# Optimization experiments

Measured on AMD Instinct MI355X. Metric: run time of the kernel, lower is better.

## Reference

```python
import jax, jax.numpy as jnp
import numpy as np

B, C, H, W = 64, 256, 64, 64
E = 4                      # num_experts
CELL = 8
OUT = CELL * CELL + 1      # 65
EPS_BN = 1e-5
EPS_LB = 1e-6


def setup_inputs() -> dict:
    key = jax.random.key(0)
    ks = jax.random.split(key, 6)
    x = jax.random.normal(ks[0], (B, C, H, W), dtype=jnp.float32)
    w_experts = jax.random.normal(ks[1], (E, C, OUT), dtype=jnp.float32) * 0.05
    b_experts = jax.random.normal(ks[2], (E, OUT), dtype=jnp.float32) * 0.05
    w_gate = jax.random.normal(ks[3], (C, E), dtype=jnp.float32) * 0.05
    b_gate = jax.random.normal(ks[4], (E,), dtype=jnp.float32) * 0.05
    gamma = jnp.ones((OUT,), dtype=jnp.float32)
    beta = jnp.zeros((OUT,), dtype=jnp.float32)
    return {"x": x, "w_experts": w_experts, "b_experts": b_experts,
            "w_gate": w_gate, "b_gate": b_gate, "gamma": gamma, "beta": beta}


def pixel_shuffle(t, r):
    n, ch, h, w = t.shape
    nc = ch // (r * r)
    t = t.reshape(n, nc, r, r, h, w)
    t = t.transpose(0, 1, 4, 2, 5, 3)
    return t.reshape(n, nc, h * r, w * r)


def reference(x, w_experts, b_experts, w_gate, b_gate, gamma, beta):
    x = jax.nn.relu(x)
    xh = x.transpose(0, 2, 3, 1)                       # [B,H,W,C]

    # gating: global-avg-pool -> linear -> softmax -> hard top-1
    pooled = xh.mean(axis=(1, 2))                      # [B,C]
    gate = jax.nn.softmax(pooled @ w_gate + b_gate, axis=-1)
    idx = jnp.argmax(gate, axis=-1)                    # [B]

    # load-balancing KL(usage || uniform)
    usage = jnp.mean(jax.nn.one_hot(idx, E, dtype=xh.dtype), axis=0) + EPS_LB
    usage = usage / usage.sum()
    lb_loss = jnp.sum(usage * (jnp.log(usage) - jnp.log(jnp.full_like(usage, 1.0 / E))))

    # fused gather->grouped-GEMM (per-sample expert weight selection)
    w_sel = w_experts[idx]                             # [B,C,OUT]
    b_sel = b_experts[idx]                             # [B,OUT]
    y = jnp.einsum('bhwc,bco->bhwo', xh, w_sel) + b_sel[:, None, None, :]
    y = y.transpose(0, 3, 1, 2)                        # [B,OUT,H,W]

    # BatchNorm2d (training mode: batch statistics, biased variance)
    mean = y.mean(axis=(0, 2, 3), keepdims=True)
    var = y.var(axis=(0, 2, 3), keepdims=True)
    logits = (y - mean) / jnp.sqrt(var + EPS_BN)
    logits = logits * gamma[None, :, None, None] + beta[None, :, None, None]

    prob = jax.nn.softmax(logits, axis=1)[:, :-1]      # drop dustbin channel
    prob = pixel_shuffle(prob, CELL)                   # [B,1,H*8,W*8]
    prob = prob[:, 0]                                  # squeeze dim=1
    return logits, prob, lb_loss
```

## Files before the change

### kernel.cpp

```cpp
#include <hip/hip_runtime.h>
#include <stdint.h>
#include <math.h>

#define B_    64
#define C_    256
#define HW_   4096
#define E_    4
#define OUT_  65
#define NPAD_ 80
#define NSPREAD_ 16

#define LOGITS_SZ (B_*OUT_*HW_)
#define PROB_SZ   (B_*512*512)

#define POOLED_OFF 0u
#define BNS_OFF    65536u
#define BNSS_OFF   70656u
#define CLEAR_BYTES 75776u
#define WT_OFF     75776u
#define YB_OFF     239616u

typedef float  f4 __attribute__((ext_vector_type(4)));
typedef short  s8 __attribute__((ext_vector_type(8)));

__device__ __forceinline__ uint32_t f2bf(float f){
  uint32_t u = __float_as_uint(f);
  return (u + 0x7FFFu + ((u >> 16) & 1u)) >> 16;
}
__device__ __forceinline__ uint32_t pk(float lo, float hi){
  return f2bf(lo) | (f2bf(hi) << 16);
}
__device__ __forceinline__ float bf2f(uint32_t u){
  return __uint_as_float((u & 0xFFFFu) << 16);
}


__global__ __launch_bounds__(256) void k_prep(const float* __restrict__ x,
                                              const float* __restrict__ w_experts,
                                              uint16_t* __restrict__ xb,
                                              uint16_t* __restrict__ Wt,
                                              float* __restrict__ pooled){
  __shared__ float pool_lds[64];
  int bid = blockIdx.x;
  int t = threadIdx.x;

  if (bid >= 8192){
    if (t >= 32) return;
    int pid = bid - 8192;
    int e = pid / NPAD_, o = pid % NPAD_;
    int ks = t >> 2, quad = t & 3;
    int c = t*8;
    float a[8];
    if (o < OUT_){
      const float* src = w_experts + (size_t)e*C_*OUT_ + o;
#pragma unroll
      for (int j = 0; j < 8; ++j) a[j] = src[(size_t)(c+j)*OUT_];
    } else {
#pragma unroll
      for (int j = 0; j < 8; ++j) a[j] = 0.f;
    }
    uint4 wv;
    wv.x = pk(a[0],a[1]); wv.y = pk(a[2],a[3]);
    wv.z = pk(a[4],a[5]); wv.w = pk(a[6],a[7]);
    uint16_t* dst = Wt + ((((size_t)(e*5 + (o>>4))*8 + ks)*64)
                          + (size_t)((o&15)*4 + quad))*8;
    *(uint4*)dst = wv;
    return;
  }

  int b = bid >> 7, ct = (bid >> 5) & 3, pt = bid & 31;
  int cg_ = t & 7, pgg = t >> 3;
  int c0 = ct*64 + cg_*8;
  int p0 = pt*128 + pgg*4;
  if (t < 64) pool_lds[t] = 0.f;
  __syncthreads();

  float v[8][4]; float s[8];
  const float* xp = x + ((size_t)(b*C_ + c0))*HW_ + p0;
#pragma unroll
  for (int r = 0; r < 8; ++r){
    float4 f = *(const float4*)(xp + (size_t)r*HW_);
    v[r][0]=fmaxf(f.x,0.f); v[r][1]=fmaxf(f.y,0.f);
    v[r][2]=fmaxf(f.z,0.f); v[r][3]=fmaxf(f.w,0.f);
    s[r] = v[r][0]+v[r][1]+v[r][2]+v[r][3];
  }
  int ksg  = ct*2 + (cg_ >> 2);
  int quad = cg_ & 3;
  uint16_t* dst0 = xb + ((((size_t)(b*256 + (p0>>4))*8 + ksg)*64)
                         + (size_t)((p0&15)*4 + quad))*8;
#pragma unroll
  for (int pp = 0; pp < 4; ++pp){
    uint4 w;
    w.x = pk(v[0][pp], v[1][pp]); w.y = pk(v[2][pp], v[3][pp]);
    w.z = pk(v[4][pp], v[5][pp]); w.w = pk(v[6][pp], v[7][pp]);
    *(uint4*)(dst0 + pp*32) = w;
  }
#pragma unroll
  for (int r = 0; r < 8; ++r){
    float vv = s[r];
    vv += __shfl_xor(vv, 8);
    vv += __shfl_xor(vv, 16);
    vv += __shfl_xor(vv, 32);
    if ((t & 56) == 0)
      atomicAdd(&pool_lds[cg_*8 + r], vv);
  }
  __syncthreads();
  if (t < 64) atomicAdd(pooled + b*C_ + ct*64 + t, pool_lds[t]);
}

__global__ __launch_bounds__(256) void k_gemm(const uint16_t* __restrict__ xb,
                                              const uint16_t* __restrict__ Wt,
                                              const float* __restrict__ pooled,
                                              const float* __restrict__ w_gate,
                                              const float* __restrict__ b_gate,
                                              const float* __restrict__ b_experts,
                                              uint16_t* __restrict__ yb,
                                              float* __restrict__ bnsum,
                                              float* __restrict__ bnss){
  __shared__ float2 bnp[NPAD_*4];
  __shared__ float glog[4];
  __shared__ int esh;
  int bid = blockIdx.x;
  int b = bid >> 5, pt = bid & 31;
  int t = threadIdx.x;
  int w = t >> 6, lane = t & 63;
  int l15 = lane & 15, quad = lane >> 4;
  int lid = l15*4 + quad;

  if (t < 4){
    float dot = 0.f;
    const float* pr = pooled + b*C_;
    for (int c = 0; c < C_; c += 4){
      float4 p4 = *(const float4*)(pr + c);
      dot += p4.x*w_gate[c*4+t] + p4.y*w_gate[(c+1)*4+t]
           + p4.z*w_gate[(c+2)*4+t] + p4.w*w_gate[(c+3)*4+t];
    }
    glog[t] = dot * (1.f/4096.f) + b_gate[t];
  }
  __syncthreads();
  if (t == 0){
    float best = glog[0]; int bi = 0;
#pragma unroll
    for (int ee = 1; ee < 4; ++ee){ float vv = glog[ee]; if (vv > best){best = vv; bi = ee;} }
    esh = bi;
  }
  __syncthreads();
  int e = esh;

  int p0 = pt*128 + w*32;
  const uint16_t* ap = xb + ((size_t)(b*256 + pt*8 + w*2))*4096 + (size_t)lid*8;
  const uint16_t* bp = Wt + (size_t)e*5*4096 + (size_t)lid*8;

  f4 acc[2][5];
#pragma unroll
  for (int mt=0; mt<2; ++mt)
#pragma unroll
    for (int nt=0; nt<5; ++nt){ f4 z = {0.f,0.f,0.f,0.f}; acc[mt][nt] = z; }

#pragma unroll
  for (int ks = 0; ks < 8; ++ks){
    s8 bv[5];
#pragma unroll
    for (int nt=0; nt<5; ++nt) bv[nt] = *(const s8*)(bp + (size_t)nt*4096 + ks*512);
#pragma unroll
    for (int mt=0; mt<2; ++mt){
      s8 av = *(const s8*)(ap + (size_t)mt*4096 + ks*512);
#pragma unroll
      for (int nt=0; nt<5; ++nt)
        acc[mt][nt] = __builtin_amdgcn_mfma_f32_16x16x32_bf16(av, bv[nt], acc[mt][nt], 0, 0, 0);
    }
  }

#pragma unroll
  for (int nt=0; nt<5; ++nt){
    int o = nt*16 + l15;
    float bias = (o < OUT_) ? b_experts[e*OUT_ + o] : 0.f;
    float s1 = 0.f, s2 = 0.f;
#pragma unroll
    for (int mt=0; mt<2; ++mt){
#pragma unroll
      for (int r=0; r<4; ++r){
        float vv = acc[mt][nt][r] + bias;
        acc[mt][nt][r] = vv;
        s1 += vv; s2 += vv*vv;
      }
      if (o < OUT_){
        size_t base = ((size_t)(b*OUT_ + o))*HW_ + p0 + mt*16 + quad*4;
        uint2 st;
        st.x = pk(acc[mt][nt][0], acc[mt][nt][1]);
        st.y = pk(acc[mt][nt][2], acc[mt][nt][3]);
        *(uint2*)(yb + base) = st;
      }
    }
    s1 += __shfl_xor(s1, 16); s1 += __shfl_xor(s1, 32);
    s2 += __shfl_xor(s2, 16); s2 += __shfl_xor(s2, 32);
    if (quad == 0) bnp[(nt*16 + l15)*4 + w] = make_float2(s1, s2);
  }
  __syncthreads();
  if (t < OUT_){
    float2 a0 = bnp[t*4+0], a1 = bnp[t*4+1], a2 = bnp[t*4+2], a3 = bnp[t*4+3];
    atomicAdd(bnsum + (bid & (NSPREAD_-1))*NPAD_ + t, a0.x+a1.x+a2.x+a3.x);
    atomicAdd(bnss  + (bid & (NSPREAD_-1))*NPAD_ + t, a0.y+a1.y+a2.y+a3.y);
  }
}

__global__ __launch_bounds__(256) void k_final(const uint16_t* __restrict__ yb,
                                               const float* __restrict__ bnsum,
                                               const float* __restrict__ bnss,
                                               const float* __restrict__ gamma,
                                               const float* __restrict__ beta,
                                               const float* __restrict__ pooled,
                                               const float* __restrict__ w_gate,
                                               const float* __restrict__ b_gate,
                                               float* __restrict__ out_logits,
                                               float* __restrict__ out_prob,
                                               float* __restrict__ out_lb){
  __shared__ float lt[OUT_*132];
  __shared__ float2 ss[OUT_];
  __shared__ float sden[256];
  __shared__ float gl[64][4];
  __shared__ int ish[64];
  int bid = blockIdx.x;
  int b = bid >> 5, pt = bid & 31;
  int p0 = pt*128;
  int t = threadIdx.x;
  if (t < OUT_){
    float s1 = 0.f, s2 = 0.f;
#pragma unroll
    for (int k = 0; k < NSPREAD_; ++k){ s1 += bnsum[k*NPAD_ + t]; s2 += bnss[k*NPAD_ + t]; }
    const float invN = 1.f/(float)(B_*HW_);
    float mean = s1*invN;
    float var  = s2*invN - mean*mean;
    float sc   = gamma[t] / sqrtf(var + 1e-5f);
    ss[t] = make_float2(sc, beta[t] - mean*sc);
  }
  __syncthreads();

  int prr = t & 15, og = t >> 4;
#pragma unroll
  for (int oi = 0; oi < 5; ++oi){
    int o = og + oi*16;
    if (o < OUT_){
      size_t base = ((size_t)(b*OUT_ + o))*HW_ + p0 + prr*8;
      uint4 raw = *(const uint4*)(yb + base);
      float f[8];
      f[0]=bf2f(raw.x); f[1]=bf2f(raw.x>>16);
      f[2]=bf2f(raw.y); f[3]=bf2f(raw.y>>16);
      f[4]=bf2f(raw.z); f[5]=bf2f(raw.z>>16);
      f[6]=bf2f(raw.w); f[7]=bf2f(raw.w>>16);
      float2 sv = ss[o];
#pragma unroll
      for (int k=0;k<8;++k) f[k] = f[k]*sv.x + sv.y;
      float4 w0 = make_float4(f[0],f[1],f[2],f[3]);
      float4 w1 = make_float4(f[4],f[5],f[6],f[7]);
      *(float4*)(out_logits + base)     = w0;
      *(float4*)(out_logits + base + 4) = w1;
      float* lp = lt + o*132 + prr*8;
      *(float4*)(lp)     = w0;
      *(float4*)(lp + 4) = w1;
    }
  }
  __syncthreads();

  int px = t & 127, hf = t >> 7;
  {
    int obeg = hf ? 33 : 0, oend = hf ? OUT_ : 33;
    float ssum = 0.f;
    for (int o = obeg; o < oend; ++o){
      float ev = __expf(lt[o*132 + px]);
      lt[o*132 + px] = ev;
      ssum += ev;
    }
    sden[hf*128 + px] = ssum;
  }
  __syncthreads();
  {
    float inv = 1.f/(sden[px] + sden[128 + px]);
    int P = p0 + px;
    int hh = P >> 6, wd = P & 63;
    float* pb = out_prob + ((size_t)b << 18) + (size_t)(hh*8)*512 + (size_t)wd*8;
#pragma unroll
    for (int r1i = 0; r1i < 4; ++r1i){
      int r1 = hf*4 + r1i;
      float4 q0, q1;
      q0.x = lt[(r1*8+0)*132+px]*inv;
      q0.y = lt[(r1*8+1)*132+px]*inv;
      q0.z = lt[(r1*8+2)*132+px]*inv;
      q0.w = lt[(r1*8+3)*132+px]*inv;
      q1.x = lt[(r1*8+4)*132+px]*inv;
      q1.y = lt[(r1*8+5)*132+px]*inv;
      q1.z = lt[(r1*8+6)*132+px]*inv;
      q1.w = lt[(r1*8+7)*132+px]*inv;
      *(float4*)(pb + (size_t)r1*512)     = q0;
      *(float4*)(pb + (size_t)r1*512 + 4) = q1;
    }
  }

  if (bid == 0){
    __syncthreads();
    int bb = t >> 2, ee = t & 3;
    float dot = 0.f;
    const float* pr = pooled + bb*C_;
    for (int c = 0; c < C_; c += 4){
      float4 p4 = *(const float4*)(pr + c);
      dot += p4.x*w_gate[c*4+ee] + p4.y*w_gate[(c+1)*4+ee]
           + p4.z*w_gate[(c+2)*4+ee] + p4.w*w_gate[(c+3)*4+ee];
    }
    gl[bb][ee] = dot * (1.f/4096.f) + b_gate[ee];
    __syncthreads();
    if (t < 64){
      float best = gl[t][0]; int bi = 0;
#pragma unroll
      for (int e2 = 1; e2 < 4; ++e2){ float vv = gl[t][e2]; if (vv > best){best = vv; bi = e2;} }
      ish[t] = bi;
    }
    __syncthreads();
    if (t == 0){
      int cnt[4] = {0,0,0,0};
      for (int b2 = 0; b2 < 64; ++b2) cnt[ish[b2]]++;
      double u[4], S = 0.0;
      for (int e2 = 0; e2 < 4; ++e2){ u[e2] = cnt[e2]/64.0 + 1e-6; S += u[e2]; }
      double lbv = 0.0;
      for (int e2 = 0; e2 < 4; ++e2){ double uu = u[e2]/S; lbv += uu*(log(uu) - log(0.25)); }
      *out_lb = (float)lbv;
    }
  }
}

extern "C" void kernel_launch(void* const* d_in, const int* in_sizes, int n_in,
                              void* d_out, int out_size, void* d_ws, size_t ws_size,
                              hipStream_t stream){
  const float* x         = (const float*)d_in[0];
  const float* w_experts = (const float*)d_in[1];
  const float* b_experts = (const float*)d_in[2];
  const float* w_gate    = (const float*)d_in[3];
  const float* b_gate    = (const float*)d_in[4];
  const float* gamma     = (const float*)d_in[5];
  const float* beta      = (const float*)d_in[6];

  float* out = (float*)d_out;
  char*  ws  = (char*)d_ws;
  float*     pooled = (float*)(ws + POOLED_OFF);
  float*     bnsum  = (float*)(ws + BNS_OFF);
  float*     bnss   = (float*)(ws + BNSS_OFF);
  uint16_t*  Wt     = (uint16_t*)(ws + WT_OFF);
  uint16_t*  ybm    = (uint16_t*)(ws + YB_OFF);
  uint16_t*  xbm    = (uint16_t*)d_out;

  float* logits = out;
  float* prob   = out + LOGITS_SZ;
  float* lbp    = out + LOGITS_SZ + PROB_SZ;

  hipMemsetAsync(ws, 0, CLEAR_BYTES, stream);
  k_prep <<<8512, 256, 0, stream>>>(x, w_experts, xbm, Wt, pooled);
  k_gemm <<<2048, 256, 0, stream>>>(xbm, Wt, pooled, w_gate, b_gate, b_experts,
                                    ybm, bnsum, bnss);
  k_final<<<2048, 256, 0, stream>>>(ybm, bnsum, bnss, gamma, beta,
                                    pooled, w_gate, b_gate, logits, prob, lbp);
}
```

Measured before the change: 488.2 us.

## Drop memset, write partial pools, nontemporal I/O, bf16 LDS staging in final

Replaces global atomic pooling with per-tile partial sums that each GEMM block reduces, so the separate memset launch can go. The BN accumulators are now zeroed inside the prep kernel. The expert choice is stored once per sample, so the final kernel no longer recomputes gating. Input loads and output stores use nontemporal hints, and the softmax staging buffer in LDS is kept as bf16 instead of fp32. Storing exponentials in bf16 lowers prob precision, and every GEMM block now reads 32 KB of partial pools.

```diff
diff --git a/kernel.cpp b/kernel.cpp
--- a/kernel.cpp
+++ b/kernel.cpp
@@ -13,12 +13,12 @@
 #define LOGITS_SZ (B_*OUT_*HW_)
 #define PROB_SZ   (B_*512*512)
 
-#define POOLED_OFF 0u
-#define BNS_OFF    65536u
-#define BNSS_OFF   70656u
-#define CLEAR_BYTES 75776u
-#define WT_OFF     75776u
-#define YB_OFF     239616u
+#define PP_OFF    0u
+#define ESEL_OFF  2097152u
+#define BNS_OFF   2097408u
+#define BNSS_OFF  2102528u
+#define WT_OFF    2107648u
+#define YB_OFF    2271488u
 
 typedef float  f4 __attribute__((ext_vector_type(4)));
 typedef short  s8 __attribute__((ext_vector_type(8)));
@@ -39,12 +39,16 @@
                                               const float* __restrict__ w_experts,
                                               uint16_t* __restrict__ xb,
                                               uint16_t* __restrict__ Wt,
-                                              float* __restrict__ pooled){
+                                              float* __restrict__ pp,
+                                              float* __restrict__ bnz){
   __shared__ float pool_lds[64];
   int bid = blockIdx.x;
   int t = threadIdx.x;
 
   if (bid >= 8192){
+    if (bid == 8192 && t >= 32){
+      for (int i = t - 32; i < 2*NSPREAD_*NPAD_; i += 224) bnz[i] = 0.f;
+    }
     if (t >= 32) return;
     int pid = bid - 8192;
     int e = pid / NPAD_, o = pid % NPAD_;
@@ -79,9 +83,9 @@
   const float* xp = x + ((size_t)(b*C_ + c0))*HW_ + p0;
 #pragma unroll
   for (int r = 0; r < 8; ++r){
-    float4 f = *(const float4*)(xp + (size_t)r*HW_);
-    v[r][0]=fmaxf(f.x,0.f); v[r][1]=fmaxf(f.y,0.f);
-    v[r][2]=fmaxf(f.z,0.f); v[r][3]=fmaxf(f.w,0.f);
+    f4 f = __builtin_nontemporal_load((const f4*)(xp + (size_t)r*HW_));
+    v[r][0]=fmaxf(f[0],0.f); v[r][1]=fmaxf(f[1],0.f);
+    v[r][2]=fmaxf(f[2],0.f); v[r][3]=fmaxf(f[3],0.f);
     s[r] = v[r][0]+v[r][1]+v[r][2]+v[r][3];
   }
   int ksg  = ct*2 + (cg_ >> 2);
@@ -89,11 +93,11 @@
   uint16_t* dst0 = xb + ((((size_t)(b*256 + (p0>>4))*8 + ksg)*64)
                          + (size_t)((p0&15)*4 + quad))*8;
 #pragma unroll
-  for (int pp = 0; pp < 4; ++pp){
+  for (int pi = 0; pi < 4; ++pi){
     uint4 w;
-    w.x = pk(v[0][pp], v[1][pp]); w.y = pk(v[2][pp], v[3][pp]);
-    w.z = pk(v[4][pp], v[5][pp]); w.w = pk(v[6][pp], v[7][pp]);
-    *(uint4*)(dst0 + pp*32) = w;
+    w.x = pk(v[0][pi], v[1][pi]); w.y = pk(v[2][pi], v[3][pi]);
+    w.z = pk(v[4][pi], v[5][pi]); w.w = pk(v[6][pi], v[7][pi]);
+    *(uint4*)(dst0 + pi*32) = w;
   }
 #pragma unroll
   for (int r = 0; r < 8; ++r){
@@ -105,20 +109,21 @@
       atomicAdd(&pool_lds[cg_*8 + r], vv);
   }
   __syncthreads();
-  if (t < 64) atomicAdd(pooled + b*C_ + ct*64 + t, pool_lds[t]);
+  if (t < 64) pp[((size_t)(b*32 + pt))*256 + ct*64 + t] = pool_lds[t];
 }
 
 __global__ __launch_bounds__(256) void k_gemm(const uint16_t* __restrict__ xb,
                                               const uint16_t* __restrict__ Wt,
-                                              const float* __restrict__ pooled,
+                                              const float* __restrict__ pp,
                                               const float* __restrict__ w_gate,
                                               const float* __restrict__ b_gate,
                                               const float* __restrict__ b_experts,
                                               uint16_t* __restrict__ yb,
                                               float* __restrict__ bnsum,
-                                              float* __restrict__ bnss){
+                                              float* __restrict__ bnss,
+                                              int* __restrict__ esel){
   __shared__ float2 bnp[NPAD_*4];
-  __shared__ float glog[4];
+  __shared__ float glp[64][4];
   __shared__ int esh;
   int bid = blockIdx.x;
   int b = bid >> 5, pt = bid & 31;
@@ -127,22 +132,31 @@
   int l15 = lane & 15, quad = lane >> 4;
   int lid = l15*4 + quad;
 
+  {
+    int ee = t & 3, cgp = t >> 2;
+    const float* ppb = pp + ((size_t)b*32)*256 + cgp*4;
+    float4 sa = make_float4(0.f,0.f,0.f,0.f);
+    for (int ptk = 0; ptk < 32; ++ptk){
+      float4 vv = *(const float4*)(ppb + ptk*256);
+      sa.x += vv.x; sa.y += vv.y; sa.z += vv.z; sa.w += vv.w;
+    }
+    int c0 = cgp*4;
+    glp[cgp][ee] = sa.x*w_gate[(c0+0)*4+ee] + sa.y*w_gate[(c0+1)*4+ee]
+                 + sa.z*w_gate[(c0+2)*4+ee] + sa.w*w_gate[(c0+3)*4+ee];
+  }
+  __syncthreads();
   if (t < 4){
-    float dot = 0.f;
-    const float* pr = pooled + b*C_;
-    for (int c = 0; c < C_; c += 4){
-      float4 p4 = *(const float4*)(pr + c);
-      dot += p4.x*w_gate[c*4+t] + p4.y*w_gate[(c+1)*4+t]
-           + p4.z*w_gate[(c+2)*4+t] + p4.w*w_gate[(c+3)*4+t];
-    }
-    glog[t] = dot * (1.f/4096.f) + b_gate[t];
+    float sg = 0.f;
+    for (int g = 0; g < 64; ++g) sg += glp[g][t];
+    glp[0][t] = sg * (1.f/4096.f) + b_gate[t];
   }
   __syncthreads();
   if (t == 0){
-    float best = glog[0]; int bi = 0;
-#pragma unroll
-    for (int ee = 1; ee < 4; ++ee){ float vv = glog[ee]; if (vv > best){best = vv; bi = ee;} }
+    float best = glp[0][0]; int bi = 0;
+#pragma unroll
+    for (int ee = 1; ee < 4; ++ee){ float vv = glp[0][ee]; if (vv > best){best = vv; bi = ee;} }
     esh = bi;
+    if (pt == 0) esel[b] = bi;
   }
   __syncthreads();
   int e = esh;
@@ -209,16 +223,13 @@
                                                const float* __restrict__ bnss,
                                                const float* __restrict__ gamma,
                                                const float* __restrict__ beta,
-                                               const float* __restrict__ pooled,
-                                               const float* __restrict__ w_gate,
-                                               const float* __restrict__ b_gate,
+                                               const int* __restrict__ esel,
                                                float* __restrict__ out_logits,
                                                float* __restrict__ out_prob,
                                                float* __restrict__ out_lb){
-  __shared__ float lt[OUT_*132];
+  __shared__ uint16_t lt[OUT_*136];
   __shared__ float2 ss[OUT_];
   __shared__ float sden[256];
-  __shared__ float gl[64][4];
   __shared__ int ish[64];
   int bid = blockIdx.x;
   int b = bid >> 5, pt = bid & 31;
@@ -251,13 +262,14 @@
       float2 sv = ss[o];
 #pragma unroll
       for (int k=0;k<8;++k) f[k] = f[k]*sv.x + sv.y;
-      float4 w0 = make_float4(f[0],f[1],f[2],f[3]);
-      float4 w1 = make_float4(f[4],f[5],f[6],f[7]);
-      *(float4*)(out_logits + base)     = w0;
-      *(float4*)(out_logits + base + 4) = w1;
-      float* lp = lt + o*132 + prr*8;
-      *(float4*)(lp)     = w0;
-      *(float4*)(lp + 4) = w1;
+      f4 w0 = {f[0],f[1],f[2],f[3]};
+      f4 w1 = {f[4],f[5],f[6],f[7]};
+      __builtin_nontemporal_store(w0, (f4*)(out_logits + base));
+      __builtin_nontemporal_store(w1, (f4*)(out_logits + base + 4));
+      uint4 st;
+      st.x = pk(f[0],f[1]); st.y = pk(f[2],f[3]);
+      st.z = pk(f[4],f[5]); st.w = pk(f[6],f[7]);
+      *(uint4*)(lt + o*136 + prr*8) = st;
     }
   }
   __syncthreads();
@@ -267,8 +279,8 @@
     int obeg = hf ? 33 : 0, oend = hf ? OUT_ : 33;
     float ssum = 0.f;
     for (int o = obeg; o < oend; ++o){
-      float ev = __expf(lt[o*132 + px]);
-      lt[o*132 + px] = ev;
+      float ev = __expf(bf2f(lt[o*136 + px]));
+      lt[o*136 + px] = (uint16_t)f2bf(ev);
       ssum += ev;
     }
     sden[hf*128 + px] = ssum;
@@ -282,38 +294,22 @@
 #pragma unroll
     for (int r1i = 0; r1i < 4; ++r1i){
       int r1 = hf*4 + r1i;
-      float4 q0, q1;
-      q0.x = lt[(r1*8+0)*132+px]*inv;
-      q0.y = lt[(r1*8+1)*132+px]*inv;
-      q0.z = lt[(r1*8+2)*132+px]*inv;
-      q0.w = lt[(r1*8+3)*132+px]*inv;
-      q1.x = lt[(r1*8+4)*132+px]*inv;
-      q1.y = lt[(r1*8+5)*132+px]*inv;
-      q1.z = lt[(r1*8+6)*132+px]*inv;
-      q1.w = lt[(r1*8+7)*132+px]*inv;
-      *(float4*)(pb + (size_t)r1*512)     = q0;
-      *(float4*)(pb + (size_t)r1*512 + 4) = q1;
+      f4 q0, q1;
+      q0[0] = bf2f(lt[(r1*8+0)*136+px])*inv;
+      q0[1] = bf2f(lt[(r1*8+1)*136+px])*inv;
+      q0[2] = bf2f(lt[(r1*8+2)*136+px])*inv;
+      q0[3] = bf2f(lt[(r1*8+3)*136+px])*inv;
+      q1[0] = bf2f(lt[(r1*8+4)*136+px])*inv;
+      q1[1] = bf2f(lt[(r1*8+5)*136+px])*inv;
+      q1[2] = bf2f(lt[(r1*8+6)*136+px])*inv;
+      q1[3] = bf2f(lt[(r1*8+7)*136+px])*inv;
+      __builtin_nontemporal_store(q0, (f4*)(pb + (size_t)r1*512));
+      __builtin_nontemporal_store(q1, (f4*)(pb + (size_t)r1*512 + 4));
     }
   }
 
   if (bid == 0){
-    __syncthreads();
-    int bb = t >> 2, ee = t & 3;
-    float dot = 0.f;
-    const float* pr = pooled + bb*C_;
-    for (int c = 0; c < C_; c += 4){
-      float4 p4 = *(const float4*)(pr + c);
-      dot += p4.x*w_gate[c*4+ee] + p4.y*w_gate[(c+1)*4+ee]
-           + p4.z*w_gate[(c+2)*4+ee] + p4.w*w_gate[(c+3)*4+ee];
-    }
-    gl[bb][ee] = dot * (1.f/4096.f) + b_gate[ee];
-    __syncthreads();
-    if (t < 64){
-      float best = gl[t][0]; int bi = 0;
-#pragma unroll
-      for (int e2 = 1; e2 < 4; ++e2){ float vv = gl[t][e2]; if (vv > best){best = vv; bi = e2;} }
-      ish[t] = bi;
-    }
+    if (t < 64) ish[t] = esel[t];
     __syncthreads();
     if (t == 0){
       int cnt[4] = {0,0,0,0};
@@ -340,7 +336,8 @@
 
   float* out = (float*)d_out;
   char*  ws  = (char*)d_ws;
-  float*     pooled = (float*)(ws + POOLED_OFF);
+  float*     pp     = (float*)(ws + PP_OFF);
+  int*       eselw  = (int*)(ws + ESEL_OFF);
   float*     bnsum  = (float*)(ws + BNS_OFF);
   float*     bnss   = (float*)(ws + BNSS_OFF);
   uint16_t*  Wt     = (uint16_t*)(ws + WT_OFF);
@@ -351,10 +348,9 @@
   float* prob   = out + LOGITS_SZ;
   float* lbp    = out + LOGITS_SZ + PROB_SZ;
 
-  hipMemsetAsync(ws, 0, CLEAR_BYTES, stream);
-  k_prep <<<8512, 256, 0, stream>>>(x, w_experts, xbm, Wt, pooled);
-  k_gemm <<<2048, 256, 0, stream>>>(xbm, Wt, pooled, w_gate, b_gate, b_experts,
-                                    ybm, bnsum, bnss);
-  k_final<<<2048, 256, 0, stream>>>(ybm, bnsum, bnss, gamma, beta,
-                                    pooled, w_gate, b_gate, logits, prob, lbp);
-}
+  k_prep <<<8512, 256, 0, stream>>>(x, w_experts, xbm, Wt, pp, bnsum);
+  k_gemm <<<2048, 256, 0, stream>>>(xbm, Wt, pp, w_gate, b_gate, b_experts,
+                                    ybm, bnsum, bnss, eselw);
+  k_final<<<2048, 256, 0, stream>>>(ybm, bnsum, bnss, gamma, beta, eselw,
+                                    logits, prob, lbp);
+}
```

Result: faster. 478.0 us (-2.1%).
